# Kernel tuning notes

Measured on AMD Instinct MI355X. Metric: run time of the kernel, lower is better.

## Reference

```python
import jax, jax.numpy as jnp
import numpy as np

PHI = (1.0 + np.sqrt(5.0)) / 2.0
B, S, D, N, L, H, V = 2, 1024, 128, 256, 2, 2, 32000


def _euler_scan(w_emb, b_emb, positions):
    # w_emb, b_emb: (B,S,D); sequential complex-rotation recurrence over S
    Bq, Sq, Dq = w_emb.shape

    def step(carry, xs):
        h_real, h_imag = carry
        w_t, b_t, pos = xs  # (B,D), (B,D), ()
        wl = 1.0 + jnp.abs(w_t)
        t_phi = pos * PHI
        th_r = h_real / wl + b_t + t_phi
        th_i = h_imag / wl + b_t + t_phi
        sr, cr = jnp.sin(th_r), jnp.cos(th_r)
        si, ci = jnp.sin(th_i), jnp.cos(th_i)
        nr = cr * ci - sr * si
        ni = cr * si + sr * ci
        return (nr, ni), (nr, ni)

    init = (jnp.zeros((Bq, Dq), w_emb.dtype), jnp.zeros((Bq, Dq), w_emb.dtype))
    xs = (jnp.swapaxes(w_emb, 0, 1), jnp.swapaxes(b_emb, 0, 1), positions)
    _, (reals, imags) = jax.lax.scan(step, init, xs)
    return jnp.swapaxes(reals, 0, 1), jnp.swapaxes(imags, 0, 1)


def _echo_head(states_real, states_imag, positions, w_q, b_q, alpha_p):
    Bq, Sq, Dq = states_real.shape
    scale = jnp.sqrt(jnp.asarray(2.0 * Dq, states_real.dtype))
    wl_q = 1.0 + jnp.abs(w_q)
    t_phi = (positions * PHI)[None, :, None]
    th_r = states_real / wl_q + b_q + t_phi
    th_i = states_imag / wl_q + b_q + t_phi
    Q = jnp.concatenate([jnp.cos(th_r), jnp.cos(th_i)], axis=-1)  # (B,S,2D)
    K = jnp.concatenate([states_real, states_imag], axis=-1)      # (B,S,2D)
    scores = jnp.einsum('bqd,bkd->bqk', Q, K) / scale
    causal = jnp.triu(jnp.ones((Sq, Sq), bool), k=1)
    scores = jnp.where(causal[None], -jnp.inf, scores)
    scores = scores.at[:, 0, 0].set(0.0)
    attn = jax.nn.softmax(scores, axis=-1)
    retrieved = jnp.einsum('bqk,bkd->bqd', attn, K)  # (B,S,2D)
    alpha = jax.nn.sigmoid(alpha_p)

    def ema_step(ema, x_t):
        ema = alpha * x_t + (1.0 - alpha) * ema
        return ema, ema

    _, ema_states = jax.lax.scan(ema_step,
                                 jnp.zeros((Bq, 2 * Dq), retrieved.dtype),
                                 jnp.swapaxes(retrieved, 0, 1))
    ema_states = jnp.swapaxes(ema_states, 0, 1)  # (B,S,2D)
    return ema_states[..., :Dq] + ema_states[..., Dq:]


def _echo_module(states_real, states_imag, positions, w_q, b_q, alpha_p, w_out, b_out):
    # w_q,b_q: (H,D); alpha_p: (H,)
    heads = jax.vmap(_echo_head, in_axes=(None, None, None, 0, 0, 0))(
        states_real, states_imag, positions, w_q, b_q, alpha_p)
    combined = heads.sum(axis=0)  # interference sum over heads
    wl_out = 1.0 + jnp.abs(w_out)
    theta = combined / wl_out + b_out
    return jnp.cos(theta) + jnp.sin(theta)


def _resonant_ffn(x, W, Bp, attn_cos, attn_sin, proj_cos, proj_sin):
    # x: (B,S,D); W,Bp,attn_*: (N,D); proj_*: (D,N)
    theta = x[..., None, :] / (1.0 + jnp.abs(W)) + Bp  # (B,S,N,D)
    cos_sum = jnp.sum(jnp.cos(theta) * attn_cos, axis=-1)  # (B,S,N)
    sin_sum = jnp.sum(jnp.sin(theta) * attn_sin, axis=-1)
    out = cos_sum @ proj_cos.T + sin_sum @ proj_sin.T  # (B,S,D)
    return jax.nn.silu(out)


def setup_inputs() -> dict:
    key = jax.random.key(0)
    ks = jax.random.split(key, 16)
    f32 = jnp.float32
    return {
        'input_ids': jax.random.randint(ks[0], (B, S), 0, V),
        'embed': jax.random.normal(ks[1], (V, 2 * D), f32) * 0.02,
        'wq': jax.random.normal(ks[2], (L, H, D), f32) * 0.02,
        'bq': jnp.zeros((L, H, D), f32),
        'alpha': jnp.full((L, H), 0.1, f32),
        'wout': jax.random.normal(ks[3], (L, D), f32) * 0.02,
        'bout': jnp.zeros((L, D), f32),
        'ffn_W': jax.random.normal(ks[4], (L, N, D), f32) * 0.02,
        'ffn_B': jnp.zeros((L, N, D), f32),
        'attn_cos': jnp.ones((L, N, D), f32),
        'attn_sin': jnp.ones((L, N, D), f32),
        'proj_cos': jax.random.uniform(ks[5], (L, D, N), f32, -0.05, 0.05),
        'proj_sin': jax.random.uniform(ks[6], (L, D, N), f32, -0.05, 0.05),
        'echo_scales': jnp.full((L,), 0.5, f32),
        'res_scales': jnp.full((L,), 0.5, f32),
        'out_proj': jax.random.normal(ks[7], (V, D), f32) * 0.02,
    }


def reference(input_ids, embed, wq, bq, alpha, wout, bout, ffn_W, ffn_B,
              attn_cos, attn_sin, proj_cos, proj_sin, echo_scales, res_scales,
              out_proj):
    emb = embed[input_ids]  # (B,S,2D)
    Dq = emb.shape[-1] // 2
    w_emb, b_emb = emb[..., :Dq], emb[..., Dq:]
    positions = jnp.arange(emb.shape[1], dtype=emb.dtype)
    sr, si = _euler_scan(w_emb, b_emb, positions)
    x = sr + si
    for l in range(wq.shape[0]):
        echo = _echo_module(sr, si, positions, wq[l], bq[l], alpha[l], wout[l], bout[l])
        res = _resonant_ffn(x, ffn_W[l], ffn_B[l], attn_cos[l], attn_sin[l],
                            proj_cos[l], proj_sin[l])
        x = x + (echo_scales[l] * echo + res_scales[l] * res)
    return x @ out_proj.T  # (B,S,V)
```

## Files before the change

kernel.cpp:

```cpp
#include <hip/hip_runtime.h>
#include <math.h>

#define B_ 2
#define S_ 1024
#define D_ 128
#define N_ 256
#define L_ 2
#define H_ 2
#define V_ 32000

#define INV2PI 0.15915494309189535f
#define PHI_F 1.61803398874989484f

__device__ __forceinline__ float fract_(float x) { return x - floorf(x); }
__device__ __forceinline__ float fsin_(float th) { return __builtin_amdgcn_sinf(fract_(th * INV2PI)); }
__device__ __forceinline__ float fcos_(float th) { return __builtin_amdgcn_cosf(fract_(th * INV2PI)); }

typedef __bf16 bf16x8 __attribute__((ext_vector_type(8)));
typedef float f32x4 __attribute__((ext_vector_type(4)));

__global__ __launch_bounds__(256) void k_gather(const int* __restrict__ ids,
                                                const float* __restrict__ embed,
                                                float* __restrict__ eg) {
    int i = blockIdx.x * 256 + threadIdx.x;
    int c = i & 255, t = (i >> 8) & 1023, b = i >> 18;
    int id = ids[b * S_ + t];
    eg[i] = embed[(size_t)id * 256 + c];
}

__global__ __launch_bounds__(128) void k_euler(const float* __restrict__ eg,
                                               float* __restrict__ sr, float* __restrict__ si,
                                               float* __restrict__ x,
                                               __bf16* __restrict__ Kh, __bf16* __restrict__ Kl) {
    int b = blockIdx.x;
    int d = threadIdx.x;
    const float* p0 = eg + (size_t)b * S_ * 256 + d;
    float h = 0.f;
    double tp = 0.0;
    const double DTP = 2.0 * 1.6180339887498949;
    const double TWO_PI = 6.283185307179586476925286766559;
    float wA[8], bA[8], wB[8], bB[8];
#pragma unroll
    for (int k = 0; k < 8; ++k) { wA[k] = p0[k * 256]; bA[k] = p0[k * 256 + 128]; }
    for (int g = 0; g < 128; ++g) {
        if (g < 127) {
            const float* p = p0 + (size_t)(g + 1) * 8 * 256;
#pragma unroll
            for (int k = 0; k < 8; ++k) { wB[k] = p[k * 256]; bB[k] = p[k * 256 + 128]; }
        }
#pragma unroll
        for (int k = 0; k < 8; ++k) {
            int t = g * 8 + k;
            float inv = 1.f / (1.f + fabsf(wA[k]));
            float th = fmaf(h, inv, 2.f * bA[k] + (float)tp);
            float u = fract_(th * INV2PI);
            float sn = __builtin_amdgcn_sinf(u);
            float cs = __builtin_amdgcn_cosf(u);
            size_t idx = ((size_t)b * S_ + t) * D_ + d;
            sr[idx] = cs; si[idx] = sn; x[idx] = cs + sn;
            size_t ki = ((size_t)b * S_ + t) * 256 + d;
            __bf16 ch = (__bf16)cs; Kh[ki] = ch; Kl[ki] = (__bf16)(cs - (float)ch);
            __bf16 sh2 = (__bf16)sn; Kh[ki + 128] = sh2; Kl[ki + 128] = (__bf16)(sn - (float)sh2);
            h = cs + sn;
            tp += DTP; if (tp >= TWO_PI) tp -= TWO_PI;
        }
#pragma unroll
        for (int k = 0; k < 8; ++k) { wA[k] = wB[k]; bA[k] = bB[k]; }
    }
}

__global__ __launch_bounds__(256) void k_ktrans(const __bf16* __restrict__ Kh, const __bf16* __restrict__ Kl,
                                                __bf16* __restrict__ KTh, __bf16* __restrict__ KTl) {
    __shared__ __bf16 th[32][34], tl[32][34];
    int b = blockIdx.z;
    int t0 = blockIdx.x * 32, d0 = blockIdx.y * 32;
    int lx = threadIdx.x & 31, ly = threadIdx.x >> 5;
#pragma unroll
    for (int i = 0; i < 4; ++i) {
        int t = t0 + ly + i * 8;
        th[ly + i * 8][lx] = Kh[((size_t)b * S_ + t) * 256 + d0 + lx];
        tl[ly + i * 8][lx] = Kl[((size_t)b * S_ + t) * 256 + d0 + lx];
    }
    __syncthreads();
#pragma unroll
    for (int i = 0; i < 4; ++i) {
        int d = d0 + ly + i * 8;
        KTh[((size_t)b * 256 + d) * S_ + t0 + lx] = th[lx][ly + i * 8];
        KTl[((size_t)b * 256 + d) * S_ + t0 + lx] = tl[lx][ly + i * 8];
    }
}

__global__ __launch_bounds__(256) void k_q(const float* __restrict__ sr, const float* __restrict__ si,
                                           const float* __restrict__ wq, const float* __restrict__ bq,
                                           __bf16* __restrict__ Qh, __bf16* __restrict__ Ql) {
    int i = blockIdx.x * 256 + threadIdx.x;
    int c = i & 255;
    int s = (i >> 8) & 1023;
    int bh = i >> 18;
    int h = bh & 1, b = bh >> 1;
    int d = c & 127;
    const float* st = (c < 128) ? sr : si;
    float v = st[((size_t)b * S_ + s) * D_ + d];
    float w = wq[h * D_ + d], bb = bq[h * D_ + d];
    float th = v / (1.f + fabsf(w)) + bb + (float)s * PHI_F;
    float qv = fcos_(th);
    __bf16 hq = (__bf16)qv;
    Qh[i] = hq; Ql[i] = (__bf16)(qv - (float)hq);
}

#define LSTR 40

__global__ __launch_bounds__(256) void k_scores_mfma(const __bf16* __restrict__ Qh, const __bf16* __restrict__ Ql,
                                                     const __bf16* __restrict__ Kh, const __bf16* __restrict__ Kl,
                                                     float* __restrict__ sc) {
    int kt = blockIdx.x, qt = blockIdx.y, bh = blockIdx.z;
    if (kt > qt) return;
    __shared__ __bf16 Ah[128 * LSTR], Al[128 * LSTR], Bh[128 * LSTR], Bl[128 * LSTR];
    int tid = threadIdx.x;
    int wid = tid >> 6, lane = tid & 63;
    int wy = wid >> 1, wx = wid & 1;
    int fl = lane & 15, qq = lane >> 4;
    int srow = tid >> 1, sseg = (tid & 1) * 16;
    const __bf16* qh = Qh + ((size_t)bh * S_ + qt * 128 + srow) * 256 + sseg;
    const __bf16* ql = Ql + ((size_t)bh * S_ + qt * 128 + srow) * 256 + sseg;
    const __bf16* kh = Kh + ((size_t)(bh >> 1) * S_ + kt * 128 + srow) * 256 + sseg;
    const __bf16* kl = Kl + ((size_t)(bh >> 1) * S_ + kt * 128 + srow) * 256 + sseg;
    int lbase = srow * LSTR + sseg;

    f32x4 acc[4][4];
#pragma unroll
    for (int i = 0; i < 4; ++i)
#pragma unroll
        for (int j = 0; j < 4; ++j) { acc[i][j][0] = 0.f; acc[i][j][1] = 0.f; acc[i][j][2] = 0.f; acc[i][j][3] = 0.f; }

    for (int kc = 0; kc < 256; kc += 32) {
        uint4 a0 = *(const uint4*)(qh + kc); uint4 a1 = *(const uint4*)(qh + kc + 8);
        uint4 l0 = *(const uint4*)(ql + kc); uint4 l1 = *(const uint4*)(ql + kc + 8);
        uint4 b0 = *(const uint4*)(kh + kc); uint4 b1 = *(const uint4*)(kh + kc + 8);
        uint4 c0 = *(const uint4*)(kl + kc); uint4 c1 = *(const uint4*)(kl + kc + 8);
        __syncthreads();
        *(uint4*)&Ah[lbase] = a0; *(uint4*)&Ah[lbase + 8] = a1;
        *(uint4*)&Al[lbase] = l0; *(uint4*)&Al[lbase + 8] = l1;
        *(uint4*)&Bh[lbase] = b0; *(uint4*)&Bh[lbase + 8] = b1;
        *(uint4*)&Bl[lbase] = c0; *(uint4*)&Bl[lbase + 8] = c1;
        __syncthreads();
        bf16x8 fah[4], fal[4], fbh[4], fbl[4];
#pragma unroll
        for (int tm = 0; tm < 4; ++tm) {
            int r = (wy * 64 + tm * 16 + fl) * LSTR + qq * 8;
            fah[tm] = *(const bf16x8*)&Ah[r];
            fal[tm] = *(const bf16x8*)&Al[r];
        }
#pragma unroll
        for (int tn = 0; tn < 4; ++tn) {
            int r = (wx * 64 + tn * 16 + fl) * LSTR + qq * 8;
            fbh[tn] = *(const bf16x8*)&Bh[r];
            fbl[tn] = *(const bf16x8*)&Bl[r];
        }
#pragma unroll
        for (int tm = 0; tm < 4; ++tm)
#pragma unroll
            for (int tn = 0; tn < 4; ++tn) {
                acc[tm][tn] = __builtin_amdgcn_mfma_f32_16x16x32_bf16(fah[tm], fbh[tn], acc[tm][tn], 0, 0, 0);
                acc[tm][tn] = __builtin_amdgcn_mfma_f32_16x16x32_bf16(fah[tm], fbl[tn], acc[tm][tn], 0, 0, 0);
                acc[tm][tn] = __builtin_amdgcn_mfma_f32_16x16x32_bf16(fal[tm], fbh[tn], acc[tm][tn], 0, 0, 0);
            }
    }
    const float s16 = 0.0625f;
    float* Cp = sc + (size_t)bh * S_ * S_;
    int grow0 = qt * 128 + wy * 64 + qq * 4;
    int gcol0 = kt * 128 + wx * 64 + fl;
#pragma unroll
    for (int tm = 0; tm < 4; ++tm)
#pragma unroll
        for (int tn = 0; tn < 4; ++tn) {
            size_t base = (size_t)(grow0 + tm * 16) * S_ + gcol0 + tn * 16;
#pragma unroll
            for (int r = 0; r < 4; ++r)
                Cp[base + (size_t)r * S_] = acc[tm][tn][r] * s16;
        }
}

__global__ __launch_bounds__(256) void k_softmax(float* __restrict__ sc) {
    int row = blockIdx.x;
    int q = row & 1023;
    float* r = sc + (size_t)row * S_;
    __bf16* rb = (__bf16*)r;
    int tid = threadIdx.x;
    __shared__ float red[256];
    float v[4];
#pragma unroll
    for (int i = 0; i < 4; ++i) {
        int k = tid + i * 256;
        v[i] = (k <= q) ? r[k] : -1e30f;
    }
    float m = fmaxf(fmaxf(v[0], v[1]), fmaxf(v[2], v[3]));
    red[tid] = m; __syncthreads();
    for (int s = 128; s > 0; s >>= 1) { if (tid < s) red[tid] = fmaxf(red[tid], red[tid + s]); __syncthreads(); }
    m = red[0]; __syncthreads();
    float e[4]; float sum = 0.f;
#pragma unroll
    for (int i = 0; i < 4; ++i) {
        int k = tid + i * 256;
        e[i] = (k <= q) ? __expf(v[i] - m) : 0.f;
        sum += e[i];
    }
    red[tid] = sum; __syncthreads();
    for (int s = 128; s > 0; s >>= 1) { if (tid < s) red[tid] += red[tid + s]; __syncthreads(); }
    float rs = 1.f / red[0];
#pragma unroll
    for (int i = 0; i < 4; ++i) {
        int k = tid + i * 256;
        if (k <= q) {
            float p = e[i] * rs;
            __bf16 h = (__bf16)p;
            rb[k] = h;
            rb[1024 + k] = (__bf16)(p - (float)h);
        }
    }
    int kz = ((q >> 7) + 1) << 7;
    for (int k = q + 1 + tid; k < kz; k += 256) { rb[k] = (__bf16)0.f; rb[1024 + k] = (__bf16)0.f; }
}

__global__ __launch_bounds__(256) void k_pv_mfma(const float* __restrict__ SCf,
                                                 const __bf16* __restrict__ KTh, const __bf16* __restrict__ KTl,
                                                 float* __restrict__ R) {
    __shared__ __bf16 Ah[128 * LSTR], Al[128 * LSTR], Bh[128 * LSTR], Bl[128 * LSTR];
    int nt = blockIdx.x, qt = blockIdx.y, bh = blockIdx.z;
    int tid = threadIdx.x;
    int wid = tid >> 6, lane = tid & 63;
    int wy = wid >> 1, wx = wid & 1;
    int fl = lane & 15, qq = lane >> 4;
    int srow = tid >> 1, sseg = (tid & 1) * 16;
    const __bf16* att = (const __bf16*)(SCf + (size_t)bh * S_ * S_);
    const __bf16* ah = att + (size_t)(qt * 128 + srow) * 2048 + sseg;
    const __bf16* al = ah + 1024;
    const __bf16* bh_p = KTh + ((size_t)(bh >> 1) * 256 + nt * 128 + srow) * S_ + sseg;
    const __bf16* bl_p = KTl + ((size_t)(bh >> 1) * 256 + nt * 128 + srow) * S_ + sseg;
    int lbase = srow * LSTR + sseg;

    f32x4 acc[4][4];
#pragma unroll
    for (int i = 0; i < 4; ++i)
#pragma unroll
        for (int j = 0; j < 4; ++j) { acc[i][j][0] = 0.f; acc[i][j][1] = 0.f; acc[i][j][2] = 0.f; acc[i][j][3] = 0.f; }

    int kmax = qt * 128 + 128;
    for (int kc = 0; kc < kmax; kc += 32) {
        uint4 a0 = *(const uint4*)(ah + kc); uint4 a1 = *(const uint4*)(ah + kc + 8);
        uint4 l0 = *(const uint4*)(al + kc); uint4 l1 = *(const uint4*)(al + kc + 8);
        uint4 b0 = *(const uint4*)(bh_p + kc); uint4 b1 = *(const uint4*)(bh_p + kc + 8);
        uint4 c0 = *(const uint4*)(bl_p + kc); uint4 c1 = *(const uint4*)(bl_p + kc + 8);
        __syncthreads();
        *(uint4*)&Ah[lbase] = a0; *(uint4*)&Ah[lbase + 8] = a1;
        *(uint4*)&Al[lbase] = l0; *(uint4*)&Al[lbase + 8] = l1;
        *(uint4*)&Bh[lbase] = b0; *(uint4*)&Bh[lbase + 8] = b1;
        *(uint4*)&Bl[lbase] = c0; *(uint4*)&Bl[lbase + 8] = c1;
        __syncthreads();
        bf16x8 fah[4], fal[4], fbh[4], fbl[4];
#pragma unroll
        for (int tm = 0; tm < 4; ++tm) {
            int r = (wy * 64 + tm * 16 + fl) * LSTR + qq * 8;
            fah[tm] = *(const bf16x8*)&Ah[r];
            fal[tm] = *(const bf16x8*)&Al[r];
        }
#pragma unroll
        for (int tn = 0; tn < 4; ++tn) {
            int r = (wx * 64 + tn * 16 + fl) * LSTR + qq * 8;
            fbh[tn] = *(const bf16x8*)&Bh[r];
            fbl[tn] = *(const bf16x8*)&Bl[r];
        }
#pragma unroll
        for (int tm = 0; tm < 4; ++tm)
#pragma unroll
            for (int tn = 0; tn < 4; ++tn) {
                acc[tm][tn] = __builtin_amdgcn_mfma_f32_16x16x32_bf16(fah[tm], fbh[tn], acc[tm][tn], 0, 0, 0);
                acc[tm][tn] = __builtin_amdgcn_mfma_f32_16x16x32_bf16(fah[tm], fbl[tn], acc[tm][tn], 0, 0, 0);
                acc[tm][tn] = __builtin_amdgcn_mfma_f32_16x16x32_bf16(fal[tm], fbh[tn], acc[tm][tn], 0, 0, 0);
            }
    }
    float* Rp = R + (size_t)bh * S_ * 256;
    int grow0 = qt * 128 + wy * 64 + qq * 4;
    int gcol0 = nt * 128 + wx * 64 + fl;
#pragma unroll
    for (int tm = 0; tm < 4; ++tm)
#pragma unroll
        for (int tn = 0; tn < 4; ++tn) {
            size_t base = (size_t)(grow0 + tm * 16) * 256 + gcol0 + tn * 16;
#pragma unroll
            for (int r = 0; r < 4; ++r)
                Rp[base + (size_t)r * 256] = acc[tm][tn][r];
        }
}

__global__ __launch_bounds__(256) void k_ema(const float* __restrict__ R,
                                             const float* __restrict__ ap,
                                             float* __restrict__ comb) {
    int blk = blockIdx.x;
    int b = blk >> 10, t = blk & 1023;
    int dim = threadIdx.x;
    __shared__ float wsh[2][64];
    __shared__ float sh[256];
    if (dim < 128) {
        int h = dim >> 6, j = dim & 63;
        float a = 1.f / (1.f + __expf(-ap[h]));
        float om = 1.f - a;
        wsh[h][j] = a * exp2f((float)j * log2f(om));
    }
    __syncthreads();
    int jmax = t < 63 ? t : 63;
    float acc = 0.f;
    for (int h = 0; h < 2; ++h) {
        const float* base = R + ((size_t)(b * 2 + h) * S_ + t) * 256 + dim;
        float s = 0.f;
        for (int j = 0; j <= jmax; ++j) s = fmaf(wsh[h][j], base[-j * 256], s);
        acc += s;
    }
    sh[dim] = acc;
    __syncthreads();
    if (dim < 128) comb[((size_t)b * S_ + t) * D_ + dim] = sh[dim] + sh[dim + 128];
}

__global__ __launch_bounds__(256) void k_prep(const float* __restrict__ W, const float* __restrict__ Bp,
                                              const float* __restrict__ ac, const float* __restrict__ as2,
                                              const float* __restrict__ pc, const float* __restrict__ ps,
                                              float* __restrict__ iwT, float* __restrict__ bpT,
                                              float* __restrict__ acT, float* __restrict__ asT,
                                              float* __restrict__ pcT, float* __restrict__ psT) {
    int i = blockIdx.x * 256 + threadIdx.x;
    int d = i & 127, n = (i >> 7) & 255, l = i >> 15;
    int ti = (l * 128 + d) * 256 + n;
    iwT[ti] = 1.f / (1.f + fabsf(W[i]));
    bpT[ti] = Bp[i];
    acT[ti] = ac[i];
    asT[ti] = as2[i];
    pcT[(l * 256 + n) * 128 + d] = pc[ti];
    psT[(l * 256 + n) * 128 + d] = ps[ti];
}

__global__ __launch_bounds__(256) void k_ffn1(const float* __restrict__ x,
                                              const float* __restrict__ iwT, const float* __restrict__ bpT,
                                              const float* __restrict__ acT, const float* __restrict__ asT,
                                              float* __restrict__ cs, float* __restrict__ ss) {
    int row0 = blockIdx.x * 8;
    int n = threadIdx.x;
    __shared__ float xs[8][128];
#pragma unroll
    for (int i = 0; i < 4; ++i) {
        int idx = n + i * 256;
        xs[idx >> 7][idx & 127] = x[(size_t)row0 * D_ + idx];
    }
    __syncthreads();
    float ac_[8] = {}, as_[8] = {};
    for (int d = 0; d < 128; ++d) {
        float iw = iwT[d * 256 + n];
        float bp = bpT[d * 256 + n];
        float wc = acT[d * 256 + n];
        float ws2 = asT[d * 256 + n];
#pragma unroll
        for (int r = 0; r < 8; ++r) {
            float th = fmaf(xs[r][d], iw, bp);
            float u = fract_(th * INV2PI);
            ac_[r] = fmaf(__builtin_amdgcn_cosf(u), wc, ac_[r]);
            as_[r] = fmaf(__builtin_amdgcn_sinf(u), ws2, as_[r]);
        }
    }
#pragma unroll
    for (int r = 0; r < 8; ++r) {
        cs[(size_t)(row0 + r) * 256 + n] = ac_[r];
        ss[(size_t)(row0 + r) * 256 + n] = as_[r];
    }
}

__global__ __launch_bounds__(128) void k_ffn2(const float* __restrict__ cs, const float* __restrict__ ss,
                                              const float* __restrict__ pcT, const float* __restrict__ psT,
                                              float* __restrict__ res) {
    int row0 = blockIdx.x * 8;
    int d = threadIdx.x;
    __shared__ float csh[8][256], ssh[8][256];
#pragma unroll
    for (int i = 0; i < 16; ++i) {
        int idx = d + i * 128;
        csh[idx >> 8][idx & 255] = cs[(size_t)row0 * 256 + idx];
        ssh[idx >> 8][idx & 255] = ss[(size_t)row0 * 256 + idx];
    }
    __syncthreads();
    float acc[8] = {};
    for (int nn = 0; nn < 256; ++nn) {
        float pc = pcT[nn * 128 + d], ps = psT[nn * 128 + d];
#pragma unroll
        for (int r = 0; r < 8; ++r)
            acc[r] = fmaf(csh[r][nn], pc, fmaf(ssh[r][nn], ps, acc[r]));
    }
#pragma unroll
    for (int r = 0; r < 8; ++r) {
        float v = acc[r];
        res[(size_t)(row0 + r) * D_ + d] = v / (1.f + __expf(-v));
    }
}

__global__ __launch_bounds__(256) void k_update(float* __restrict__ x, const float* __restrict__ comb,
                                                const float* __restrict__ res,
                                                const float* __restrict__ wout, const float* __restrict__ bout,
                                                const float* __restrict__ esp, const float* __restrict__ rsp) {
    int i = blockIdx.x * 256 + threadIdx.x;
    int d = i & 127;
    float wl = 1.f + fabsf(wout[d]);
    float th = comb[i] / wl + bout[d];
    float u = fract_(th * INV2PI);
    float echo = __builtin_amdgcn_cosf(u) + __builtin_amdgcn_sinf(u);
    x[i] += esp[0] * echo + rsp[0] * res[i];
}

__global__ __launch_bounds__(256) void k_cvt(const float* __restrict__ X, const float* __restrict__ P,
                                             __bf16* __restrict__ Xh, __bf16* __restrict__ Xl,
                                             __bf16* __restrict__ Ph, __bf16* __restrict__ Pl) {
    int i = blockIdx.x * 256 + threadIdx.x;
    const int NX = 2048 * 128;
    float v; __bf16 *h, *l; int j;
    if (i < NX) { v = X[i]; h = Xh; l = Xl; j = i; }
    else { v = P[i - NX]; h = Ph; l = Pl; j = i - NX; }
    __bf16 hi = (__bf16)v;
    float lo = v - (float)hi;
    h[j] = hi;
    l[j] = (__bf16)lo;
}

__global__ __launch_bounds__(256) void k_out_mfma(const __bf16* __restrict__ Xh, const __bf16* __restrict__ Xl,
                                                  const __bf16* __restrict__ Ph, const __bf16* __restrict__ Pl,
                                                  float* __restrict__ out) {
    __shared__ __bf16 Ah[128 * LSTR], Al[128 * LSTR], Bh[128 * LSTR], Bl[128 * LSTR];
    int mt = blockIdx.x, nt = blockIdx.y;
    int tid = threadIdx.x;
    int wid = tid >> 6, lane = tid & 63;
    int wy = wid >> 1, wx = wid & 1;
    int fl = lane & 15, q = lane >> 4;
    int srow = tid >> 1, sseg = (tid & 1) * 16;
    const __bf16* xh = Xh + (size_t)(mt * 128 + srow) * 128 + sseg;
    const __bf16* xl = Xl + (size_t)(mt * 128 + srow) * 128 + sseg;
    const __bf16* ph = Ph + (size_t)(nt * 128 + srow) * 128 + sseg;
    const __bf16* pl = Pl + (size_t)(nt * 128 + srow) * 128 + sseg;
    int lbase = srow * LSTR + sseg;

    f32x4 acc[4][4];
#pragma unroll
    for (int i = 0; i < 4; ++i)
#pragma unroll
        for (int j = 0; j < 4; ++j) { acc[i][j][0] = 0.f; acc[i][j][1] = 0.f; acc[i][j][2] = 0.f; acc[i][j][3] = 0.f; }

    for (int kc = 0; kc < 128; kc += 32) {
        uint4 vxh0 = *(const uint4*)(xh + kc); uint4 vxh1 = *(const uint4*)(xh + kc + 8);
        uint4 vxl0 = *(const uint4*)(xl + kc); uint4 vxl1 = *(const uint4*)(xl + kc + 8);
        uint4 vph0 = *(const uint4*)(ph + kc); uint4 vph1 = *(const uint4*)(ph + kc + 8);
        uint4 vpl0 = *(const uint4*)(pl + kc); uint4 vpl1 = *(const uint4*)(pl + kc + 8);
        __syncthreads();
        *(uint4*)&Ah[lbase] = vxh0; *(uint4*)&Ah[lbase + 8] = vxh1;
        *(uint4*)&Al[lbase] = vxl0; *(uint4*)&Al[lbase + 8] = vxl1;
        *(uint4*)&Bh[lbase] = vph0; *(uint4*)&Bh[lbase + 8] = vph1;
        *(uint4*)&Bl[lbase] = vpl0; *(uint4*)&Bl[lbase + 8] = vpl1;
        __syncthreads();
        bf16x8 ah[4], al[4], bh[4], bl[4];
#pragma unroll
        for (int tm = 0; tm < 4; ++tm) {
            int r = (wy * 64 + tm * 16 + fl) * LSTR + q * 8;
            ah[tm] = *(const bf16x8*)&Ah[r];
            al[tm] = *(const bf16x8*)&Al[r];
        }
#pragma unroll
        for (int tn = 0; tn < 4; ++tn) {
            int r = (wx * 64 + tn * 16 + fl) * LSTR + q * 8;
            bh[tn] = *(const bf16x8*)&Bh[r];
            bl[tn] = *(const bf16x8*)&Bl[r];
        }
#pragma unroll
        for (int tm = 0; tm < 4; ++tm)
#pragma unroll
            for (int tn = 0; tn < 4; ++tn) {
                acc[tm][tn] = __builtin_amdgcn_mfma_f32_16x16x32_bf16(ah[tm], bh[tn], acc[tm][tn], 0, 0, 0);
                acc[tm][tn] = __builtin_amdgcn_mfma_f32_16x16x32_bf16(ah[tm], bl[tn], acc[tm][tn], 0, 0, 0);
                acc[tm][tn] = __builtin_amdgcn_mfma_f32_16x16x32_bf16(al[tm], bh[tn], acc[tm][tn], 0, 0, 0);
            }
    }
    int grow0 = mt * 128 + wy * 64 + q * 4;
    int gcol0 = nt * 128 + wx * 64 + fl;
#pragma unroll
    for (int tm = 0; tm < 4; ++tm)
#pragma unroll
        for (int tn = 0; tn < 4; ++tn) {
            size_t base = (size_t)(grow0 + tm * 16) * V_ + gcol0 + tn * 16;
#pragma unroll
            for (int r = 0; r < 4; ++r)
                out[base + (size_t)r * V_] = acc[tm][tn][r];
        }
}

extern "C" void kernel_launch(void* const* d_in, const int* in_sizes, int n_in,
                              void* d_out, int out_size, void* d_ws, size_t ws_size,
                              hipStream_t stream) {
    const int* ids = (const int*)d_in[0];
    const float* embed = (const float*)d_in[1];
    const float* wq = (const float*)d_in[2];
    const float* bq = (const float*)d_in[3];
    const float* alpha = (const float*)d_in[4];
    const float* wout = (const float*)d_in[5];
    const float* bout = (const float*)d_in[6];
    const float* ffnW = (const float*)d_in[7];
    const float* ffnB = (const float*)d_in[8];
    const float* acos_ = (const float*)d_in[9];
    const float* asin_ = (const float*)d_in[10];
    const float* pcos = (const float*)d_in[11];
    const float* psin = (const float*)d_in[12];
    const float* escl = (const float*)d_in[13];
    const float* rscl = (const float*)d_in[14];
    const float* oprj = (const float*)d_in[15];
    float* out = (float*)d_out;
    float* ws = (float*)d_ws;

    float* EG = ws;
    float* SR = EG + 524288;
    float* SI = SR + 262144;
    float* X  = SI + 262144;
    float* KB = X + 262144;
    float* Q  = KB + 524288;
    float* SC = Q + 1048576;
    float* RT = SC + 4194304;
    float* CB = RT + 1048576;
    float* CS = CB + 262144;
    float* SS = CS + 524288;
    float* RS = SS + 524288;
    float* T_IW = RS + 262144;
    float* T_BP = T_IW + 65536;
    float* T_AC = T_BP + 65536;
    float* T_AS = T_AC + 65536;
    float* T_PC = T_AS + 65536;
    float* T_PS = T_PC + 65536;
    __bf16* KH = (__bf16*)KB;
    __bf16* KL = KH + 524288;
    __bf16* QH = (__bf16*)Q;
    __bf16* QL = QH + 1048576;
    __bf16* KTH = (__bf16*)EG;
    __bf16* KTL = KTH + 524288;
    __bf16* XH = (__bf16*)Q;
    __bf16* XL = XH + 262144;
    __bf16* PH = XL + 262144;
    __bf16* PL = PH + 4096000;

    k_prep<<<256, 256, 0, stream>>>(ffnW, ffnB, acos_, asin_, pcos, psin,
                                    T_IW, T_BP, T_AC, T_AS, T_PC, T_PS);
    k_gather<<<2048, 256, 0, stream>>>(ids, embed, EG);
    k_euler<<<2, 128, 0, stream>>>(EG, SR, SI, X, KH, KL);
    k_ktrans<<<dim3(32, 8, 2), 256, 0, stream>>>(KH, KL, KTH, KTL);

    for (int l = 0; l < L_; ++l) {
        k_q<<<4096, 256, 0, stream>>>(SR, SI, wq + l * H_ * D_, bq + l * H_ * D_, QH, QL);
        k_scores_mfma<<<dim3(8, 8, 4), 256, 0, stream>>>(QH, QL, KH, KL, SC);
        k_softmax<<<4096, 256, 0, stream>>>(SC);
        k_pv_mfma<<<dim3(2, 8, 4), 256, 0, stream>>>(SC, KTH, KTL, RT);
        k_ema<<<2048, 256, 0, stream>>>(RT, alpha + l * H_, CB);
        k_ffn1<<<256, 256, 0, stream>>>(X, T_IW + l * 32768, T_BP + l * 32768,
                                        T_AC + l * 32768, T_AS + l * 32768, CS, SS);
        k_ffn2<<<256, 128, 0, stream>>>(CS, SS, T_PC + l * 32768, T_PS + l * 32768, RS);
        k_update<<<1024, 256, 0, stream>>>(X, CB, RS, wout + l * D_, bout + l * D_,
                                           escl + l, rscl + l);
    }
    k_cvt<<<17024, 256, 0, stream>>>(X, oprj, XH, XL, PH, PL);
    k_out_mfma<<<dim3(16, 250), 256, 0, stream>>>(XH, XL, PH, PL, out);
}
```

Before: 935.7 us.

## Fuse softmax into PV, merge EMA/FFN/update tail, and fold conversions

Several kernels are merged. Gather runs with weight prep, the Euler scan writes the transposed K directly, and Q is computed for both layers in one launch. Softmax is folded into the PV kernel, which computes row max and sum itself and builds the probability operands on the fly. EMA, both FFN stages and the update become one tail kernel that also emits the split-bf16 X for the last layer. The output GEMM converts out_proj from fp32 inside the kernel. The aim is fewer launches and fewer intermediate global round-trips, at the cost of recomputing exp in PV for each column tile and converting the projection per block.

```diff
diff --git a/kernel.cpp b/kernel.cpp
--- a/kernel.cpp
+++ b/kernel.cpp
@@ -19,19 +19,37 @@
 typedef __bf16 bf16x8 __attribute__((ext_vector_type(8)));
 typedef float f32x4 __attribute__((ext_vector_type(4)));
 
-__global__ __launch_bounds__(256) void k_gather(const int* __restrict__ ids,
-                                                const float* __restrict__ embed,
-                                                float* __restrict__ eg) {
-    int i = blockIdx.x * 256 + threadIdx.x;
-    int c = i & 255, t = (i >> 8) & 1023, b = i >> 18;
-    int id = ids[b * S_ + t];
-    eg[i] = embed[(size_t)id * 256 + c];
+__global__ __launch_bounds__(256) void k_gp(const int* __restrict__ ids, const float* __restrict__ embed,
+                                            float* __restrict__ eg,
+                                            const float* __restrict__ W, const float* __restrict__ Bp,
+                                            const float* __restrict__ ac, const float* __restrict__ as2,
+                                            const float* __restrict__ pc, const float* __restrict__ ps,
+                                            float* __restrict__ iwT, float* __restrict__ bpT,
+                                            float* __restrict__ acT, float* __restrict__ asT,
+                                            float* __restrict__ pcT, float* __restrict__ psT) {
+    int blk = blockIdx.x;
+    if (blk < 2048) {
+        int i = blk * 256 + threadIdx.x;
+        int c = i & 255, t = (i >> 8) & 1023, b = i >> 18;
+        eg[i] = embed[(size_t)ids[b * S_ + t] * 256 + c];
+    } else {
+        int i = (blk - 2048) * 256 + threadIdx.x;
+        int d = i & 127, n = (i >> 7) & 255, l = i >> 15;
+        int ti = (l * 128 + d) * 256 + n;
+        iwT[ti] = 1.f / (1.f + fabsf(W[i]));
+        bpT[ti] = Bp[i];
+        acT[ti] = ac[i];
+        asT[ti] = as2[i];
+        pcT[(l * 256 + n) * 128 + d] = pc[ti];
+        psT[(l * 256 + n) * 128 + d] = ps[ti];
+    }
 }
 
 __global__ __launch_bounds__(128) void k_euler(const float* __restrict__ eg,
                                                float* __restrict__ sr, float* __restrict__ si,
                                                float* __restrict__ x,
-                                               __bf16* __restrict__ Kh, __bf16* __restrict__ Kl) {
+                                               __bf16* __restrict__ Kh, __bf16* __restrict__ Kl,
+                                               __bf16* __restrict__ KTh, __bf16* __restrict__ KTl) {
     int b = blockIdx.x;
     int d = threadIdx.x;
     const float* p0 = eg + (size_t)b * S_ * 256 + d;
@@ -58,9 +76,15 @@
             float cs = __builtin_amdgcn_cosf(u);
             size_t idx = ((size_t)b * S_ + t) * D_ + d;
             sr[idx] = cs; si[idx] = sn; x[idx] = cs + sn;
+            __bf16 ch = (__bf16)cs; __bf16 cl = (__bf16)(cs - (float)ch);
+            __bf16 sh2 = (__bf16)sn; __bf16 sl = (__bf16)(sn - (float)sh2);
             size_t ki = ((size_t)b * S_ + t) * 256 + d;
-            __bf16 ch = (__bf16)cs; Kh[ki] = ch; Kl[ki] = (__bf16)(cs - (float)ch);
-            __bf16 sh2 = (__bf16)sn; Kh[ki + 128] = sh2; Kl[ki + 128] = (__bf16)(sn - (float)sh2);
+            Kh[ki] = ch; Kl[ki] = cl;
+            Kh[ki + 128] = sh2; Kl[ki + 128] = sl;
+            size_t kt1 = ((size_t)b * 256 + d) * S_ + t;
+            size_t kt2 = ((size_t)b * 256 + d + 128) * S_ + t;
+            KTh[kt1] = ch; KTl[kt1] = cl;
+            KTh[kt2] = sh2; KTl[kt2] = sl;
             h = cs + sn;
             tp += DTP; if (tp >= TWO_PI) tp -= TWO_PI;
         }
@@ -69,43 +93,27 @@
     }
 }
 
-__global__ __launch_bounds__(256) void k_ktrans(const __bf16* __restrict__ Kh, const __bf16* __restrict__ Kl,
-                                                __bf16* __restrict__ KTh, __bf16* __restrict__ KTl) {
-    __shared__ __bf16 th[32][34], tl[32][34];
-    int b = blockIdx.z;
-    int t0 = blockIdx.x * 32, d0 = blockIdx.y * 32;
-    int lx = threadIdx.x & 31, ly = threadIdx.x >> 5;
-#pragma unroll
-    for (int i = 0; i < 4; ++i) {
-        int t = t0 + ly + i * 8;
-        th[ly + i * 8][lx] = Kh[((size_t)b * S_ + t) * 256 + d0 + lx];
-        tl[ly + i * 8][lx] = Kl[((size_t)b * S_ + t) * 256 + d0 + lx];
-    }
-    __syncthreads();
-#pragma unroll
-    for (int i = 0; i < 4; ++i) {
-        int d = d0 + ly + i * 8;
-        KTh[((size_t)b * 256 + d) * S_ + t0 + lx] = th[lx][ly + i * 8];
-        KTl[((size_t)b * 256 + d) * S_ + t0 + lx] = tl[lx][ly + i * 8];
-    }
-}
-
-__global__ __launch_bounds__(256) void k_q(const float* __restrict__ sr, const float* __restrict__ si,
-                                           const float* __restrict__ wq, const float* __restrict__ bq,
-                                           __bf16* __restrict__ Qh, __bf16* __restrict__ Ql) {
+__global__ __launch_bounds__(256) void k_qq(const float* __restrict__ sr, const float* __restrict__ si,
+                                            const float* __restrict__ wq, const float* __restrict__ bq,
+                                            __bf16* __restrict__ Qh0, __bf16* __restrict__ Ql0,
+                                            __bf16* __restrict__ Qh1, __bf16* __restrict__ Ql1) {
     int i = blockIdx.x * 256 + threadIdx.x;
-    int c = i & 255;
-    int s = (i >> 8) & 1023;
-    int bh = i >> 18;
+    int l = i >> 20;
+    int j = i & 0xFFFFF;
+    int c = j & 255;
+    int s = (j >> 8) & 1023;
+    int bh = j >> 18;
     int h = bh & 1, b = bh >> 1;
     int d = c & 127;
     const float* st = (c < 128) ? sr : si;
     float v = st[((size_t)b * S_ + s) * D_ + d];
-    float w = wq[h * D_ + d], bb = bq[h * D_ + d];
+    float w = wq[(l * H_ + h) * D_ + d], bb = bq[(l * H_ + h) * D_ + d];
     float th = v / (1.f + fabsf(w)) + bb + (float)s * PHI_F;
     float qv = fcos_(th);
     __bf16 hq = (__bf16)qv;
-    Qh[i] = hq; Ql[i] = (__bf16)(qv - (float)hq);
+    __bf16 lq = (__bf16)(qv - (float)hq);
+    if (l == 0) { Qh0[j] = hq; Ql0[j] = lq; }
+    else        { Qh1[j] = hq; Ql1[j] = lq; }
 }
 
 #define LSTR 40
@@ -181,60 +189,48 @@
         }
 }
 
-__global__ __launch_bounds__(256) void k_softmax(float* __restrict__ sc) {
-    int row = blockIdx.x;
-    int q = row & 1023;
-    float* r = sc + (size_t)row * S_;
-    __bf16* rb = (__bf16*)r;
-    int tid = threadIdx.x;
-    __shared__ float red[256];
-    float v[4];
-#pragma unroll
-    for (int i = 0; i < 4; ++i) {
-        int k = tid + i * 256;
-        v[i] = (k <= q) ? r[k] : -1e30f;
-    }
-    float m = fmaxf(fmaxf(v[0], v[1]), fmaxf(v[2], v[3]));
-    red[tid] = m; __syncthreads();
-    for (int s = 128; s > 0; s >>= 1) { if (tid < s) red[tid] = fmaxf(red[tid], red[tid + s]); __syncthreads(); }
-    m = red[0]; __syncthreads();
-    float e[4]; float sum = 0.f;
-#pragma unroll
-    for (int i = 0; i < 4; ++i) {
-        int k = tid + i * 256;
-        e[i] = (k <= q) ? __expf(v[i] - m) : 0.f;
-        sum += e[i];
-    }
-    red[tid] = sum; __syncthreads();
-    for (int s = 128; s > 0; s >>= 1) { if (tid < s) red[tid] += red[tid + s]; __syncthreads(); }
-    float rs = 1.f / red[0];
-#pragma unroll
-    for (int i = 0; i < 4; ++i) {
-        int k = tid + i * 256;
-        if (k <= q) {
-            float p = e[i] * rs;
-            __bf16 h = (__bf16)p;
-            rb[k] = h;
-            rb[1024 + k] = (__bf16)(p - (float)h);
-        }
-    }
-    int kz = ((q >> 7) + 1) << 7;
-    for (int k = q + 1 + tid; k < kz; k += 256) { rb[k] = (__bf16)0.f; rb[1024 + k] = (__bf16)0.f; }
-}
-
-__global__ __launch_bounds__(256) void k_pv_mfma(const float* __restrict__ SCf,
-                                                 const __bf16* __restrict__ KTh, const __bf16* __restrict__ KTl,
-                                                 float* __restrict__ R) {
+__global__ __launch_bounds__(256) void k_pv_sm(const float* __restrict__ SCf,
+                                               const __bf16* __restrict__ KTh, const __bf16* __restrict__ KTl,
+                                               float* __restrict__ R) {
     __shared__ __bf16 Ah[128 * LSTR], Al[128 * LSTR], Bh[128 * LSTR], Bl[128 * LSTR];
+    __shared__ float mrow[128], rrow[128];
     int nt = blockIdx.x, qt = blockIdx.y, bh = blockIdx.z;
     int tid = threadIdx.x;
     int wid = tid >> 6, lane = tid & 63;
     int wy = wid >> 1, wx = wid & 1;
     int fl = lane & 15, qq = lane >> 4;
-    int srow = tid >> 1, sseg = (tid & 1) * 16;
-    const __bf16* att = (const __bf16*)(SCf + (size_t)bh * S_ * S_);
-    const __bf16* ah = att + (size_t)(qt * 128 + srow) * 2048 + sseg;
-    const __bf16* al = ah + 1024;
+    int srow = tid >> 1, half = tid & 1, sseg = half * 16;
+    const float* Sp = SCf + (size_t)bh * S_ * S_;
+    int kceil = qt * 128 + 128;
+    {
+        int r = srow;
+        int q = qt * 128 + r;
+        const float* rp = Sp + (size_t)q * S_;
+        float m = -3e38f;
+        for (int c = half * 4; c < kceil; c += 8) {
+            float4 v = *(const float4*)&rp[c];
+            if (c + 0 <= q) m = fmaxf(m, v.x);
+            if (c + 1 <= q) m = fmaxf(m, v.y);
+            if (c + 2 <= q) m = fmaxf(m, v.z);
+            if (c + 3 <= q) m = fmaxf(m, v.w);
+        }
+        m = fmaxf(m, __shfl_xor(m, 1));
+        float s = 0.f;
+        for (int c = half * 4; c < kceil; c += 8) {
+            float4 v = *(const float4*)&rp[c];
+            if (c + 0 <= q) s += __expf(v.x - m);
+            if (c + 1 <= q) s += __expf(v.y - m);
+            if (c + 2 <= q) s += __expf(v.z - m);
+            if (c + 3 <= q) s += __expf(v.w - m);
+        }
+        s += __shfl_xor(s, 1);
+        mrow[r] = m;
+        rrow[r] = 1.f / s;
+    }
+    __syncthreads();
+    float mR = mrow[srow], rsR = rrow[srow];
+    int qrow = qt * 128 + srow;
+    const float* ap = Sp + (size_t)qrow * S_ + sseg;
     const __bf16* bh_p = KTh + ((size_t)(bh >> 1) * 256 + nt * 128 + srow) * S_ + sseg;
     const __bf16* bl_p = KTl + ((size_t)(bh >> 1) * 256 + nt * 128 + srow) * S_ + sseg;
     int lbase = srow * LSTR + sseg;
@@ -245,15 +241,28 @@
 #pragma unroll
         for (int j = 0; j < 4; ++j) { acc[i][j][0] = 0.f; acc[i][j][1] = 0.f; acc[i][j][2] = 0.f; acc[i][j][3] = 0.f; }
 
-    int kmax = qt * 128 + 128;
-    for (int kc = 0; kc < kmax; kc += 32) {
-        uint4 a0 = *(const uint4*)(ah + kc); uint4 a1 = *(const uint4*)(ah + kc + 8);
-        uint4 l0 = *(const uint4*)(al + kc); uint4 l1 = *(const uint4*)(al + kc + 8);
+    for (int kc = 0; kc < kceil; kc += 32) {
+        float4 f0 = *(const float4*)(ap + kc);
+        float4 f1 = *(const float4*)(ap + kc + 4);
+        float4 f2 = *(const float4*)(ap + kc + 8);
+        float4 f3 = *(const float4*)(ap + kc + 12);
         uint4 b0 = *(const uint4*)(bh_p + kc); uint4 b1 = *(const uint4*)(bh_p + kc + 8);
         uint4 c0 = *(const uint4*)(bl_p + kc); uint4 c1 = *(const uint4*)(bl_p + kc + 8);
+        float vv[16] = {f0.x, f0.y, f0.z, f0.w, f1.x, f1.y, f1.z, f1.w,
+                        f2.x, f2.y, f2.z, f2.w, f3.x, f3.y, f3.z, f3.w};
+        bf16x8 h0, h1, l0, l1;
+#pragma unroll
+        for (int e = 0; e < 16; ++e) {
+            int col = kc + sseg + e;
+            float p = (col <= qrow) ? __expf(vv[e] - mR) * rsR : 0.f;
+            __bf16 hi = (__bf16)p;
+            __bf16 lo = (__bf16)(p - (float)hi);
+            if (e < 8) { h0[e] = hi; l0[e] = lo; }
+            else       { h1[e - 8] = hi; l1[e - 8] = lo; }
+        }
         __syncthreads();
-        *(uint4*)&Ah[lbase] = a0; *(uint4*)&Ah[lbase + 8] = a1;
-        *(uint4*)&Al[lbase] = l0; *(uint4*)&Al[lbase + 8] = l1;
+        *(bf16x8*)&Ah[lbase] = h0; *(bf16x8*)&Ah[lbase + 8] = h1;
+        *(bf16x8*)&Al[lbase] = l0; *(bf16x8*)&Al[lbase + 8] = l1;
         *(uint4*)&Bh[lbase] = b0; *(uint4*)&Bh[lbase + 8] = b1;
         *(uint4*)&Bl[lbase] = c0; *(uint4*)&Bl[lbase + 8] = c1;
         __syncthreads();
@@ -293,141 +302,123 @@
         }
 }
 
-__global__ __launch_bounds__(256) void k_ema(const float* __restrict__ R,
-                                             const float* __restrict__ ap,
-                                             float* __restrict__ comb) {
-    int blk = blockIdx.x;
-    int b = blk >> 10, t = blk & 1023;
-    int dim = threadIdx.x;
-    __shared__ float wsh[2][64];
-    __shared__ float sh[256];
-    if (dim < 128) {
-        int h = dim >> 6, j = dim & 63;
-        float a = 1.f / (1.f + __expf(-ap[h]));
-        float om = 1.f - a;
-        wsh[h][j] = a * exp2f((float)j * log2f(om));
-    }
-    __syncthreads();
-    int jmax = t < 63 ? t : 63;
-    float acc = 0.f;
-    for (int h = 0; h < 2; ++h) {
-        const float* base = R + ((size_t)(b * 2 + h) * S_ + t) * 256 + dim;
-        float s = 0.f;
-        for (int j = 0; j <= jmax; ++j) s = fmaf(wsh[h][j], base[-j * 256], s);
-        acc += s;
-    }
-    sh[dim] = acc;
-    __syncthreads();
-    if (dim < 128) comb[((size_t)b * S_ + t) * D_ + dim] = sh[dim] + sh[dim + 128];
-}
-
-__global__ __launch_bounds__(256) void k_prep(const float* __restrict__ W, const float* __restrict__ Bp,
-                                              const float* __restrict__ ac, const float* __restrict__ as2,
-                                              const float* __restrict__ pc, const float* __restrict__ ps,
-                                              float* __restrict__ iwT, float* __restrict__ bpT,
-                                              float* __restrict__ acT, float* __restrict__ asT,
-                                              float* __restrict__ pcT, float* __restrict__ psT) {
-    int i = blockIdx.x * 256 + threadIdx.x;
-    int d = i & 127, n = (i >> 7) & 255, l = i >> 15;
-    int ti = (l * 128 + d) * 256 + n;
-    iwT[ti] = 1.f / (1.f + fabsf(W[i]));
-    bpT[ti] = Bp[i];
-    acT[ti] = ac[i];
-    asT[ti] = as2[i];
-    pcT[(l * 256 + n) * 128 + d] = pc[ti];
-    psT[(l * 256 + n) * 128 + d] = ps[ti];
-}
-
-__global__ __launch_bounds__(256) void k_ffn1(const float* __restrict__ x,
+#define TROWS 4
+__global__ __launch_bounds__(256) void k_tail(const float* __restrict__ R,
+                                              const float* __restrict__ apar,
+                                              float* __restrict__ x,
                                               const float* __restrict__ iwT, const float* __restrict__ bpT,
                                               const float* __restrict__ acT, const float* __restrict__ asT,
-                                              float* __restrict__ cs, float* __restrict__ ss) {
-    int row0 = blockIdx.x * 8;
-    int n = threadIdx.x;
-    __shared__ float xs[8][128];
-#pragma unroll
-    for (int i = 0; i < 4; ++i) {
-        int idx = n + i * 256;
-        xs[idx >> 7][idx & 127] = x[(size_t)row0 * D_ + idx];
+                                              const float* __restrict__ pcT, const float* __restrict__ psT,
+                                              const float* __restrict__ wout, const float* __restrict__ bout,
+                                              const float* __restrict__ esp, const float* __restrict__ rsp,
+                                              __bf16* __restrict__ Xh, __bf16* __restrict__ Xl, int last) {
+    int blk = blockIdx.x;
+    int row0 = blk * TROWS;
+    int b = row0 >> 10, t0 = row0 & 1023;
+    int tid = threadIdx.x;
+    __shared__ float wsh[2][64];
+    __shared__ float emah[TROWS][256];
+    __shared__ float xs[TROWS][128];
+    __shared__ float csh[TROWS][256], ssh[TROWS][256];
+    if (tid < 128) {
+        int h = tid >> 6, j = tid & 63;
+        float a = 1.f / (1.f + __expf(-apar[h]));
+        wsh[h][j] = a * exp2f((float)j * log2f(1.f - a));
+    }
+    {
+        int i0 = tid;
+        xs[i0 >> 7][i0 & 127] = x[(size_t)row0 * D_ + i0];
+        int i1 = tid + 256;
+        xs[i1 >> 7][i1 & 127] = x[(size_t)row0 * D_ + i1];
     }
     __syncthreads();
-    float ac_[8] = {}, as_[8] = {};
-    for (int d = 0; d < 128; ++d) {
-        float iw = iwT[d * 256 + n];
-        float bp = bpT[d * 256 + n];
-        float wc = acT[d * 256 + n];
-        float ws2 = asT[d * 256 + n];
-#pragma unroll
-        for (int r = 0; r < 8; ++r) {
-            float th = fmaf(xs[r][d], iw, bp);
+    {
+        int dim = tid;
+        if (t0 >= 63) {
+#pragma unroll
+            for (int r = 0; r < TROWS; ++r) {
+                int t = t0 + r;
+                float acc = 0.f;
+#pragma unroll
+                for (int h = 0; h < 2; ++h) {
+                    const float* base = R + ((size_t)(b * 2 + h) * S_ + t) * 256 + dim;
+                    float s = 0.f;
+#pragma unroll
+                    for (int j = 0; j < 64; ++j) s = fmaf(wsh[h][j], base[-j * 256], s);
+                    acc += s;
+                }
+                emah[r][dim] = acc;
+            }
+        } else {
+            for (int r = 0; r < TROWS; ++r) {
+                int t = t0 + r;
+                int jm = t < 63 ? t : 63;
+                float acc = 0.f;
+                for (int h = 0; h < 2; ++h) {
+                    const float* base = R + ((size_t)(b * 2 + h) * S_ + t) * 256 + dim;
+                    float s = 0.f;
+                    for (int j = 0; j <= jm; ++j) s = fmaf(wsh[h][j], base[-j * 256], s);
+                    acc += s;
+                }
+                emah[r][dim] = acc;
+            }
+        }
+    }
+    __syncthreads();
+    {
+        int n = tid;
+        float ac_[TROWS] = {}, as_[TROWS] = {};
+        for (int d = 0; d < 128; ++d) {
+            float iw = iwT[d * 256 + n];
+            float bp = bpT[d * 256 + n];
+            float wc = acT[d * 256 + n];
+            float ws2 = asT[d * 256 + n];
+#pragma unroll
+            for (int r = 0; r < TROWS; ++r) {
+                float th = fmaf(xs[r][d], iw, bp);
+                float u = fract_(th * INV2PI);
+                ac_[r] = fmaf(__builtin_amdgcn_cosf(u), wc, ac_[r]);
+                as_[r] = fmaf(__builtin_amdgcn_sinf(u), ws2, as_[r]);
+            }
+        }
+#pragma unroll
+        for (int r = 0; r < TROWS; ++r) { csh[r][n] = ac_[r]; ssh[r][n] = as_[r]; }
+    }
+    __syncthreads();
+    {
+        int g = tid >> 7, d = tid & 127;
+        float a0 = 0.f, a1 = 0.f;
+        for (int nn = 0; nn < 256; ++nn) {
+            float pc = pcT[nn * 128 + d], ps = psT[nn * 128 + d];
+            a0 = fmaf(csh[g * 2 + 0][nn], pc, fmaf(ssh[g * 2 + 0][nn], ps, a0));
+            a1 = fmaf(csh[g * 2 + 1][nn], pc, fmaf(ssh[g * 2 + 1][nn], ps, a1));
+        }
+        float es = esp[0], rs = rsp[0];
+        float wl = 1.f + fabsf(wout[d]);
+        float bo = bout[d];
+#pragma unroll
+        for (int rr = 0; rr < 2; ++rr) {
+            int r = g * 2 + rr;
+            float v = rr ? a1 : a0;
+            float res = v / (1.f + __expf(-v));
+            float comb = emah[r][d] + emah[r][d + 128];
+            float th = comb / wl + bo;
             float u = fract_(th * INV2PI);
-            ac_[r] = fmaf(__builtin_amdgcn_cosf(u), wc, ac_[r]);
-            as_[r] = fmaf(__builtin_amdgcn_sinf(u), ws2, as_[r]);
-        }
-    }
-#pragma unroll
-    for (int r = 0; r < 8; ++r) {
-        cs[(size_t)(row0 + r) * 256 + n] = ac_[r];
-        ss[(size_t)(row0 + r) * 256 + n] = as_[r];
-    }
-}
-
-__global__ __launch_bounds__(128) void k_ffn2(const float* __restrict__ cs, const float* __restrict__ ss,
-                                              const float* __restrict__ pcT, const float* __restrict__ psT,
-                                              float* __restrict__ res) {
-    int row0 = blockIdx.x * 8;
-    int d = threadIdx.x;
-    __shared__ float csh[8][256], ssh[8][256];
-#pragma unroll
-    for (int i = 0; i < 16; ++i) {
-        int idx = d + i * 128;
-        csh[idx >> 8][idx & 255] = cs[(size_t)row0 * 256 + idx];
-        ssh[idx >> 8][idx & 255] = ss[(size_t)row0 * 256 + idx];
-    }
-    __syncthreads();
-    float acc[8] = {};
-    for (int nn = 0; nn < 256; ++nn) {
-        float pc = pcT[nn * 128 + d], ps = psT[nn * 128 + d];
-#pragma unroll
-        for (int r = 0; r < 8; ++r)
-            acc[r] = fmaf(csh[r][nn], pc, fmaf(ssh[r][nn], ps, acc[r]));
-    }
-#pragma unroll
-    for (int r = 0; r < 8; ++r) {
-        float v = acc[r];
-        res[(size_t)(row0 + r) * D_ + d] = v / (1.f + __expf(-v));
-    }
-}
-
-__global__ __launch_bounds__(256) void k_update(float* __restrict__ x, const float* __restrict__ comb,
-                                                const float* __restrict__ res,
-                                                const float* __restrict__ wout, const float* __restrict__ bout,
-                                                const float* __restrict__ esp, const float* __restrict__ rsp) {
-    int i = blockIdx.x * 256 + threadIdx.x;
-    int d = i & 127;
-    float wl = 1.f + fabsf(wout[d]);
-    float th = comb[i] / wl + bout[d];
-    float u = fract_(th * INV2PI);
-    float echo = __builtin_amdgcn_cosf(u) + __builtin_amdgcn_sinf(u);
-    x[i] += esp[0] * echo + rsp[0] * res[i];
-}
-
-__global__ __launch_bounds__(256) void k_cvt(const float* __restrict__ X, const float* __restrict__ P,
-                                             __bf16* __restrict__ Xh, __bf16* __restrict__ Xl,
-                                             __bf16* __restrict__ Ph, __bf16* __restrict__ Pl) {
-    int i = blockIdx.x * 256 + threadIdx.x;
-    const int NX = 2048 * 128;
-    float v; __bf16 *h, *l; int j;
-    if (i < NX) { v = X[i]; h = Xh; l = Xl; j = i; }
-    else { v = P[i - NX]; h = Ph; l = Pl; j = i - NX; }
-    __bf16 hi = (__bf16)v;
-    float lo = v - (float)hi;
-    h[j] = hi;
-    l[j] = (__bf16)lo;
+            float echo = __builtin_amdgcn_cosf(u) + __builtin_amdgcn_sinf(u);
+            size_t gi = (size_t)(row0 + r) * D_ + d;
+            float xn = xs[r][d] + es * echo + rs * res;
+            x[gi] = xn;
+            if (last) {
+                __bf16 hi = (__bf16)xn;
+                Xh[gi] = hi;
+                Xl[gi] = (__bf16)(xn - (float)hi);
+            }
+        }
+    }
 }
 
 __global__ __launch_bounds__(256) void k_out_mfma(const __bf16* __restrict__ Xh, const __bf16* __restrict__ Xl,
-                                                  const __bf16* __restrict__ Ph, const __bf16* __restrict__ Pl,
+                                                  const float* __restrict__ P,
                                                   float* __restrict__ out) {
     __shared__ __bf16 Ah[128 * LSTR], Al[128 * LSTR], Bh[128 * LSTR], Bl[128 * LSTR];
     int mt = blockIdx.x, nt = blockIdx.y;
@@ -438,8 +429,7 @@
     int srow = tid >> 1, sseg = (tid & 1) * 16;
     const __bf16* xh = Xh + (size_t)(mt * 128 + srow) * 128 + sseg;
     const __bf16* xl = Xl + (size_t)(mt * 128 + srow) * 128 + sseg;
-    const __bf16* ph = Ph + (size_t)(nt * 128 + srow) * 128 + sseg;
-    const __bf16* pl = Pl + (size_t)(nt * 128 + srow) * 128 + sseg;
+    const float* pf = P + (size_t)(nt * 128 + srow) * 128 + sseg;
     int lbase = srow * LSTR + sseg;
 
     f32x4 acc[4][4];
@@ -451,13 +441,25 @@
     for (int kc = 0; kc < 128; kc += 32) {
         uint4 vxh0 = *(const uint4*)(xh + kc); uint4 vxh1 = *(const uint4*)(xh + kc + 8);
         uint4 vxl0 = *(const uint4*)(xl + kc); uint4 vxl1 = *(const uint4*)(xl + kc + 8);
-        uint4 vph0 = *(const uint4*)(ph + kc); uint4 vph1 = *(const uint4*)(ph + kc + 8);
-        uint4 vpl0 = *(const uint4*)(pl + kc); uint4 vpl1 = *(const uint4*)(pl + kc + 8);
+        float4 p0 = *(const float4*)(pf + kc);
+        float4 p1 = *(const float4*)(pf + kc + 4);
+        float4 p2 = *(const float4*)(pf + kc + 8);
+        float4 p3 = *(const float4*)(pf + kc + 12);
+        float pv_[16] = {p0.x, p0.y, p0.z, p0.w, p1.x, p1.y, p1.z, p1.w,
+                         p2.x, p2.y, p2.z, p2.w, p3.x, p3.y, p3.z, p3.w};
+        bf16x8 bh0, bh1, bl0, bl1;
+#pragma unroll
+        for (int e = 0; e < 16; ++e) {
+            __bf16 hi = (__bf16)pv_[e];
+            __bf16 lo = (__bf16)(pv_[e] - (float)hi);
+            if (e < 8) { bh0[e] = hi; bl0[e] = lo; }
+            else       { bh1[e - 8] = hi; bl1[e - 8] = lo; }
+        }
         __syncthreads();
         *(uint4*)&Ah[lbase] = vxh0; *(uint4*)&Ah[lbase + 8] = vxh1;
         *(uint4*)&Al[lbase] = vxl0; *(uint4*)&Al[lbase + 8] = vxl1;
-        *(uint4*)&Bh[lbase] = vph0; *(uint4*)&Bh[lbase + 8] = vph1;
-        *(uint4*)&Bl[lbase] = vpl0; *(uint4*)&Bl[lbase + 8] = vpl1;
+        *(bf16x8*)&Bh[lbase] = bh0; *(bf16x8*)&Bh[lbase + 8] = bh1;
+        *(bf16x8*)&Bl[lbase] = bl0; *(bf16x8*)&Bl[lbase + 8] = bl1;
         __syncthreads();
         bf16x8 ah[4], al[4], bh[4], bl[4];
 #pragma unroll
@@ -521,14 +523,12 @@
     float* SI = SR + 262144;
     float* X  = SI + 262144;
     float* KB = X + 262144;
-    float* Q  = KB + 524288;
-    float* SC = Q + 1048576;
+    float* Q0 = KB + 524288;
+    float* SC = Q0 + 1048576;
     float* RT = SC + 4194304;
-    float* CB = RT + 1048576;
-    float* CS = CB + 262144;
-    float* SS = CS + 524288;
-    float* RS = SS + 524288;
-    float* T_IW = RS + 262144;
+    float* KT = RT + 1048576;
+    float* Q1 = KT + 524288;
+    float* T_IW = Q1 + 1048576;
     float* T_BP = T_IW + 65536;
     float* T_AC = T_BP + 65536;
     float* T_AS = T_AC + 65536;
@@ -536,33 +536,29 @@
     float* T_PS = T_PC + 65536;
     __bf16* KH = (__bf16*)KB;
     __bf16* KL = KH + 524288;
-    __bf16* QH = (__bf16*)Q;
-    __bf16* QL = QH + 1048576;
-    __bf16* KTH = (__bf16*)EG;
+    __bf16* QH0 = (__bf16*)Q0;
+    __bf16* QL0 = QH0 + 1048576;
+    __bf16* QH1 = (__bf16*)Q1;
+    __bf16* QL1 = QH1 + 1048576;
+    __bf16* KTH = (__bf16*)KT;
     __bf16* KTL = KTH + 524288;
-    __bf16* XH = (__bf16*)Q;
+    __bf16* XH = (__bf16*)SC;
     __bf16* XL = XH + 262144;
-    __bf16* PH = XL + 262144;
-    __bf16* PL = PH + 4096000;
-
-    k_prep<<<256, 256, 0, stream>>>(ffnW, ffnB, acos_, asin_, pcos, psin,
-                                    T_IW, T_BP, T_AC, T_AS, T_PC, T_PS);
-    k_gather<<<2048, 256, 0, stream>>>(ids, embed, EG);
-    k_euler<<<2, 128, 0, stream>>>(EG, SR, SI, X, KH, KL);
-    k_ktrans<<<dim3(32, 8, 2), 256, 0, stream>>>(KH, KL, KTH, KTL);
+
+    k_gp<<<2304, 256, 0, stream>>>(ids, embed, EG, ffnW, ffnB, acos_, asin_, pcos, psin,
+                                   T_IW, T_BP, T_AC, T_AS, T_PC, T_PS);
+    k_euler<<<2, 128, 0, stream>>>(EG, SR, SI, X, KH, KL, KTH, KTL);
+    k_qq<<<8192, 256, 0, stream>>>(SR, SI, wq, bq, QH0, QL0, QH1, QL1);
 
     for (int l = 0; l < L_; ++l) {
-        k_q<<<4096, 256, 0, stream>>>(SR, SI, wq + l * H_ * D_, bq + l * H_ * D_, QH, QL);
-        k_scores_mfma<<<dim3(8, 8, 4), 256, 0, stream>>>(QH, QL, KH, KL, SC);
-        k_softmax<<<4096, 256, 0, stream>>>(SC);
-        k_pv_mfma<<<dim3(2, 8, 4), 256, 0, stream>>>(SC, KTH, KTL, RT);
-        k_ema<<<2048, 256, 0, stream>>>(RT, alpha + l * H_, CB);
-        k_ffn1<<<256, 256, 0, stream>>>(X, T_IW + l * 32768, T_BP + l * 32768,
-                                        T_AC + l * 32768, T_AS + l * 32768, CS, SS);
-        k_ffn2<<<256, 128, 0, stream>>>(CS, SS, T_PC + l * 32768, T_PS + l * 32768, RS);
-        k_update<<<1024, 256, 0, stream>>>(X, CB, RS, wout + l * D_, bout + l * D_,
-                                           escl + l, rscl + l);
-    }
-    k_cvt<<<17024, 256, 0, stream>>>(X, oprj, XH, XL, PH, PL);
-    k_out_mfma<<<dim3(16, 250), 256, 0, stream>>>(XH, XL, PH, PL, out);
-}
+        k_scores_mfma<<<dim3(8, 8, 4), 256, 0, stream>>>(l ? QH1 : QH0, l ? QL1 : QL0, KH, KL, SC);
+        k_pv_sm<<<dim3(2, 8, 4), 256, 0, stream>>>(SC, KTH, KTL, RT);
+        k_tail<<<512, 256, 0, stream>>>(RT, alpha + l * H_, X,
+                                        T_IW + l * 32768, T_BP + l * 32768,
+                                        T_AC + l * 32768, T_AS + l * 32768,
+                                        T_PC + l * 32768, T_PS + l * 32768,
+                                        wout + l * D_, bout + l * D_,
+                                        escl + l, rscl + l, XH, XL, l == L_ - 1);
+    }
+    k_out_mfma<<<dim3(16, 250), 256, 0, stream>>>(XH, XL, oprj, out);
+}
```

New measurement: 901.4 us. -3.7%, faster.
